# Kernel tuning notes

Measured on AMD Instinct MI355X. Metric: run time of the kernel, lower is better.

## Reference

```python
import jax, jax.numpy as jnp
import numpy as np

DIM = 1024      # input_size (C)
E = 8           # num_experts
TOPK = 2        # use_experts
MLP = 4 * DIM   # int(dim * mlp_ratio)
B, N = 4, 1024


def _gelu(v):
    # torch nn.GELU default = exact erf gelu
    return jax.nn.gelu(v, approximate=False)


def setup_inputs() -> dict:
    key = jax.random.key(0)
    ks = jax.random.split(key, 20)
    s = 0.02
    f32 = jnp.float32
    return {
        "x": jax.random.normal(ks[0], (B, N, DIM), f32),
        "prompt": jax.random.normal(ks[1], (B, N, DIM), f32),
        "t": jax.random.uniform(ks[2], (B, N, 1), f32) * 1000.0,
        # gating time_embedding MLP
        "te_w1": jax.random.normal(ks[3], (1, DIM), f32) * s,
        "te_b1": jnp.zeros((DIM,), f32),
        "te_w2": jax.random.normal(ks[4], (DIM, DIM), f32) * s,
        "te_b2": jnp.zeros((DIM,), f32),
        "gate_w": jax.random.normal(ks[5], (3 * DIM, E), f32) * s,
        # stacked per-expert params [E, ...]
        "ex_tw1": jax.random.normal(ks[6], (E, 1, DIM), f32) * s,
        "ex_tb1": jnp.zeros((E, DIM), f32),
        "ex_tw2": jax.random.normal(ks[7], (E, DIM, DIM), f32) * s,
        "ex_tb2": jnp.zeros((E, DIM), f32),
        "ex_mw1": jax.random.normal(ks[8], (E, 2 * DIM, MLP), f32) * s,
        "ex_mb1": jnp.zeros((E, MLP), f32),
        "ex_mw2": jax.random.normal(ks[9], (E, MLP, DIM), f32) * s,
        "ex_mb2": jnp.zeros((E, DIM), f32),
    }


def _forward(x, prompt, t, te_w1, te_b1, te_w2, te_b2, gate_w,
             ex_tw1, ex_tb1, ex_tw2, ex_tb2, ex_mw1, ex_mb1, ex_mw2, ex_mb2):
    Bb, Nn, C = x.shape
    xf = x.reshape(-1, C)            # [T, C]
    pf = prompt.reshape(-1, C)
    tf = t.reshape(-1, 1)            # [T, 1]
    T = xf.shape[0]

    # noisy_gate (eval: no noise)
    t_emb = _gelu(tf @ te_w1 + te_b1) @ te_w2 + te_b2          # [T, C]
    x_cat = jnp.concatenate([xf, pf, t_emb], axis=-1)          # [T, 3C]
    logits = x_cat @ gate_w                                    # [T, E]
    top_l, top_i = jax.lax.top_k(logits, TOPK)
    gates = jnp.zeros_like(logits).at[
        jnp.arange(T)[:, None], top_i
    ].set(jax.nn.softmax(top_l, axis=1))                       # [T, E]

    # per-expert diffusion MLP, dense over experts (gate==0 contributes 0,
    # identical math to dispatch/split/index_add combine)
    te = _gelu(jnp.einsum('to,eod->etd', tf, ex_tw1) + ex_tb1[:, None, :])
    te = jnp.einsum('etd,edf->etf', te, ex_tw2) + ex_tb2[:, None, :]   # [E,T,C]
    xc = jnp.concatenate([jnp.broadcast_to(xf, (E, T, C)), te], axis=-1)  # [E,T,2C]
    h = _gelu(jnp.einsum('etc,ech->eth', xc, ex_mw1) + ex_mb1[:, None, :])
    out_e = jnp.einsum('eth,ehd->etd', h, ex_mw2) + ex_mb2[:, None, :]    # [E,T,C]

    out_f = jnp.einsum('te,etd->td', gates, out_e)             # combine
    output = out_f.reshape(Bb, Nn, C)

    load = gates.sum(0)                                        # [E]
    eps = 1e-10
    bal = jnp.var(load, ddof=1) / (jnp.mean(load) ** 2 + eps)
    moe_loss = bal + bal  # weight_balance + load_balance (same argument)
    return output, moe_loss


def reference(x, prompt, t, te_w1, te_b1, te_w2, te_b2, gate_w,
              ex_tw1, ex_tb1, ex_tw2, ex_tb2, ex_mw1, ex_mb1, ex_mw2, ex_mb2):
    return _forward(x, prompt, t, te_w1, te_b1, te_w2, te_b2, gate_w,
                    ex_tw1, ex_tb1, ex_tw2, ex_tb2, ex_mw1, ex_mb1, ex_mw2, ex_mb2)
```

## Files before the change

kernel.cpp:

```cpp
#include <hip/hip_runtime.h>
#include <cmath>

#define TTOK 4096
#define CDIM 1024
#define NE 8
#define MLPD 4096
#define PCAP (2*TTOK + NE*128)

typedef __attribute__((ext_vector_type(8))) short short8;
typedef __attribute__((ext_vector_type(4))) float float4v;

__device__ __forceinline__ float bf2f(unsigned short h){
  return __uint_as_float(((unsigned int)h) << 16);
}
__device__ __forceinline__ unsigned short f2bf(float f){
  unsigned int u = __float_as_uint(f);
  u += 0x7FFFu + ((u >> 16) & 1u);
  return (unsigned short)(u >> 16);
}
__device__ __forceinline__ float gelu_exact(float x){
  return 0.5f * x * (1.0f + erff(x * 0.70710678118654752f));
}
__device__ __forceinline__ void gld16(const void* g, void* l){
  __builtin_amdgcn_global_load_lds((const __attribute__((address_space(1))) void*)g,
                                   (__attribute__((address_space(3))) void*)l, 16, 0, 0);
}

__global__ __launch_bounds__(256) void k_zero(float* out, int n, int* counts, float* loadsum){
  int i = blockIdx.x*256 + threadIdx.x;
  if (i < n) out[i] = 0.f;
  if (i < NE){ counts[i] = 0; loadsum[i] = 0.f; }
}

__global__ __launch_bounds__(256) void k_m2(const float* __restrict__ te_w2,
    const float* __restrict__ te_b2, const float* __restrict__ gate_w,
    float* __restrict__ M2, float* __restrict__ c2){
  int idx = blockIdx.x*256 + threadIdx.x;
  if (idx < CDIM*NE){
    int i = idx >> 3, e = idx & 7;
    float s = 0.f;
    for (int j = 0; j < CDIM; j++)
      s += te_w2[(size_t)i*CDIM + j] * gate_w[(size_t)(2*CDIM + j)*NE + e];
    M2[idx] = s;
  } else if (idx < CDIM*NE + NE){
    int e = idx - CDIM*NE;
    float s = 0.f;
    for (int j = 0; j < CDIM; j++)
      s += te_b2[j] * gate_w[(size_t)(2*CDIM + j)*NE + e];
    c2[e] = s;
  }
}

__global__ __launch_bounds__(256) void k_cvt_x(const float* __restrict__ x,
                                               unsigned short* __restrict__ xb, int n4){
  int i = blockIdx.x*256 + threadIdx.x;
  if (i >= n4) return;
  float4 v = reinterpret_cast<const float4*>(x)[i];
  ushort4 o;
  o.x = f2bf(v.x); o.y = f2bf(v.y); o.z = f2bf(v.z); o.w = f2bf(v.w);
  reinterpret_cast<ushort4*>(xb)[i] = o;
}

__global__ __launch_bounds__(256) void k_cvt_w(const float* __restrict__ W,
    unsigned short* __restrict__ Wt, int K, int N){
  __shared__ float tile[32][33];
  int kb = blockIdx.x*32, nb = blockIdx.y*32, e = blockIdx.z;
  const float* Wp = W + (size_t)e*K*N;
  unsigned short* Wo = Wt + (size_t)e*K*N;
  int tx = threadIdx.x & 31, ty = threadIdx.x >> 5;
  #pragma unroll
  for (int i = 0; i < 32; i += 8)
    tile[ty+i][tx] = Wp[(size_t)(kb+ty+i)*N + nb + tx];
  __syncthreads();
  #pragma unroll
  for (int i = 0; i < 32; i += 8)
    Wo[(size_t)(nb+ty+i)*K + kb + tx] = f2bf(tile[tx][ty+i]);
}

__global__ __launch_bounds__(256) void k_gate(const float* __restrict__ x,
    const float* __restrict__ p, const float* __restrict__ t,
    const float* __restrict__ te_w1, const float* __restrict__ te_b1,
    const float* __restrict__ gate_w, const float* __restrict__ M2,
    const float* __restrict__ c2,
    int* __restrict__ ti, float* __restrict__ tg,
    int* __restrict__ counts, float* __restrict__ loadsum){
  int tok = blockIdx.x, tid = threadIdx.x;
  float tv = t[tok];
  float acc[NE];
  #pragma unroll
  for (int e = 0; e < NE; e++) acc[e] = 0.f;
  for (int j = tid; j < CDIM; j += 256){
    float xv = x[(size_t)tok*CDIM + j];
    float pv = p[(size_t)tok*CDIM + j];
    float vv = gelu_exact(tv*te_w1[j] + te_b1[j]);
    const float* g0 = gate_w + (size_t)j*NE;
    const float* g1 = gate_w + (size_t)(CDIM + j)*NE;
    const float* m2 = M2 + (size_t)j*NE;
    #pragma unroll
    for (int e = 0; e < NE; e++) acc[e] += xv*g0[e] + pv*g1[e] + vv*m2[e];
  }
  __shared__ float red[256][NE];
  #pragma unroll
  for (int e = 0; e < NE; e++) red[tid][e] = acc[e];
  __syncthreads();
  for (int s = 128; s > 0; s >>= 1){
    if (tid < s){
      #pragma unroll
      for (int e = 0; e < NE; e++) red[tid][e] += red[tid+s][e];
    }
    __syncthreads();
  }
  if (tid == 0){
    float lg[NE];
    #pragma unroll
    for (int e = 0; e < NE; e++) lg[e] = red[0][e] + c2[e];
    int i1 = 0; float l1 = lg[0];
    #pragma unroll
    for (int e = 1; e < NE; e++) if (lg[e] > l1){ l1 = lg[e]; i1 = e; }
    int i2 = -1; float l2 = -3.4e38f;
    #pragma unroll
    for (int e = 0; e < NE; e++) if (e != i1 && lg[e] > l2){ l2 = lg[e]; i2 = e; }
    float ex  = expf(l2 - l1);
    float g1v = 1.f/(1.f + ex);
    float g2v = ex/(1.f + ex);
    ti[tok*2]   = i1; ti[tok*2+1] = i2;
    tg[tok*2]   = g1v; tg[tok*2+1] = g2v;
    atomicAdd(&counts[i1], 1);  atomicAdd(&counts[i2], 1);
    atomicAdd(&loadsum[i1], g1v); atomicAdd(&loadsum[i2], g2v);
  }
}

__global__ __launch_bounds__(256) void k_scan(const int* __restrict__ counts,
    int* __restrict__ poff, int* __restrict__ fillpos,
    int* __restrict__ tok_id, float* __restrict__ pgate, int* __restrict__ pe, int padg){
  __shared__ int so[NE+1];
  __shared__ int sc[NE];
  if (threadIdx.x == 0){
    int o = 0;
    for (int e = 0; e < NE; e++){
      so[e] = o; poff[e] = o; fillpos[e] = o;
      sc[e] = counts[e];
      o += (sc[e] + padg - 1) & ~(padg - 1);
    }
    so[NE] = o; poff[NE] = o;
  }
  __syncthreads();
  for (int e = 0; e < NE; e++){
    int s = so[e] + sc[e], en = so[e+1];
    for (int i = s + (int)threadIdx.x; i < en; i += 256){
      tok_id[i] = 0; pgate[i] = 0.f; pe[i] = e;
    }
  }
}

__global__ __launch_bounds__(256) void k_fill(const int* __restrict__ ti,
    const float* __restrict__ tg, int* __restrict__ fillpos,
    int* __restrict__ tok_id, float* __restrict__ pgate, int* __restrict__ pe){
  int tok = blockIdx.x*256 + threadIdx.x;
  if (tok >= TTOK) return;
  #pragma unroll
  for (int k = 0; k < 2; k++){
    int e = ti[tok*2 + k];
    int pos = atomicAdd(&fillpos[e], 1);
    tok_id[pos] = tok;
    pgate[pos]  = tg[tok*2 + k];
    pe[pos]     = e;
  }
}

__global__ __launch_bounds__(256) void k_vgelu(const float* __restrict__ t,
    const float* __restrict__ tw1, const float* __restrict__ tb1,
    const int* __restrict__ tok_id, const int* __restrict__ pe,
    const int* __restrict__ poff, unsigned short* __restrict__ vbuf){
  int idx = blockIdx.x*256 + threadIdx.x;
  int r = idx >> 10, k = idx & (CDIM - 1);
  if (r >= poff[NE]) return;
  int e = pe[r];
  float tv = t[tok_id[r]];
  float u = tv * tw1[(size_t)e*CDIM + k] + tb1[(size_t)e*CDIM + k];
  vbuf[(size_t)r*CDIM + k] = f2bf(gelu_exact(u));
}


__global__ __launch_bounds__(256,2) void k_mfma_te(
    const unsigned short* __restrict__ vbuf,
    const unsigned short* __restrict__ Wt1, const float* __restrict__ tb2,
    const int* __restrict__ poff, const int* __restrict__ pe,
    unsigned short* __restrict__ tebuf){
  __shared__ unsigned short As[128*32];
  __shared__ unsigned short Bs[128*32];
  int r0 = blockIdx.y * 128;
  if (r0 >= poff[NE]) return;
  int e = pe[r0];
  int n0 = blockIdx.x * 128;
  int tid = threadIdx.x, lane = tid & 63, w = tid >> 6;
  const unsigned short* Bp = Wt1 + (size_t)e*CDIM*CDIM;
  int mb = (w&1)*64, nb = (w>>1)*64;
  float4v acc[4][4];
  #pragma unroll
  for (int i=0;i<4;i++)
    #pragma unroll
    for (int j=0;j<4;j++) acc[i][j] = (float4v){0.f,0.f,0.f,0.f};
  int rowA = w*32 + (lane>>2);
  int ck = (lane&3)*8;
  for (int k0 = 0; k0 < CDIM; k0 += 32){
    __syncthreads();
    unsigned short* lA = As + (w*32)*32;
    unsigned short* lB = Bs + (w*32)*32;
    gld16(vbuf + (size_t)(r0+rowA)*CDIM + k0 + ck, lA);
    gld16(vbuf + (size_t)(r0+rowA+16)*CDIM + k0 + ck, lA + 16*32);
    gld16(Bp + (size_t)(n0+rowA)*CDIM + k0 + ck, lB);
    gld16(Bp + (size_t)(n0+rowA+16)*CDIM + k0 + ck, lB + 16*32);
    __syncthreads();
    short8 a[4], b[4];
    #pragma unroll
    for (int mi=0;mi<4;mi++) a[mi] = *(const short8*)(As + (mb+mi*16+(lane&15))*32 + (lane>>4)*8);
    #pragma unroll
    for (int ni=0;ni<4;ni++) b[ni] = *(const short8*)(Bs + (nb+ni*16+(lane&15))*32 + (lane>>4)*8);
    #pragma unroll
    for (int mi=0;mi<4;mi++)
      #pragma unroll
      for (int ni=0;ni<4;ni++)
        acc[mi][ni] = __builtin_amdgcn_mfma_f32_16x16x32_bf16(a[mi], b[ni], acc[mi][ni], 0, 0, 0);
  }
  int col = lane & 15, rq = (lane>>4)*4;
  const float* bias = tb2 + (size_t)e*CDIM + n0;
  #pragma unroll
  for (int mi=0;mi<4;mi++)
    #pragma unroll
    for (int ni=0;ni<4;ni++){
      int n = nb + ni*16 + col;
      #pragma unroll
      for (int rg=0;rg<4;rg++){
        int r = r0 + mb + mi*16 + rq + rg;
        tebuf[(size_t)r*CDIM + n0 + n] = f2bf(acc[mi][ni][rg] + bias[n]);
      }
    }
}

__global__ __launch_bounds__(256,2) void k_mfma_h(
    const unsigned short* __restrict__ xb, const unsigned short* __restrict__ tebuf,
    const unsigned short* __restrict__ Wt2, const float* __restrict__ mb1,
    const int* __restrict__ poff, const int* __restrict__ pe,
    const int* __restrict__ tok_id, unsigned short* __restrict__ hbuf){
  __shared__ unsigned short As[128*32];
  __shared__ unsigned short Bs[128*32];
  __shared__ int toks[128];
  int r0 = blockIdx.y * 128;
  if (r0 >= poff[NE]) return;
  int e = pe[r0];
  int n0 = blockIdx.x * 128;
  int tid = threadIdx.x, lane = tid & 63, w = tid >> 6;
  if (tid < 128) toks[tid] = tok_id[r0 + tid];
  const unsigned short* Bp = Wt2 + (size_t)e*(2*CDIM)*MLPD;
  int mb = (w&1)*64, nb = (w>>1)*64;
  float4v acc[4][4];
  #pragma unroll
  for (int i=0;i<4;i++)
    #pragma unroll
    for (int j=0;j<4;j++) acc[i][j] = (float4v){0.f,0.f,0.f,0.f};
  int rowA = w*32 + (lane>>2);
  int ck = (lane&3)*8;
  for (int k0 = 0; k0 < 2*CDIM; k0 += 32){
    __syncthreads();
    unsigned short* lA = As + (w*32)*32;
    unsigned short* lB = Bs + (w*32)*32;
    if (k0 < CDIM){
      int tok0 = toks[rowA], tok1 = toks[rowA+16];
      gld16(xb + (size_t)tok0*CDIM + k0 + ck, lA);
      gld16(xb + (size_t)tok1*CDIM + k0 + ck, lA + 16*32);
    } else {
      gld16(tebuf + (size_t)(r0+rowA)*CDIM + (k0-CDIM) + ck, lA);
      gld16(tebuf + (size_t)(r0+rowA+16)*CDIM + (k0-CDIM) + ck, lA + 16*32);
    }
    gld16(Bp + (size_t)(n0+rowA)*(2*CDIM) + k0 + ck, lB);
    gld16(Bp + (size_t)(n0+rowA+16)*(2*CDIM) + k0 + ck, lB + 16*32);
    __syncthreads();
    short8 a[4], b[4];
    #pragma unroll
    for (int mi=0;mi<4;mi++) a[mi] = *(const short8*)(As + (mb+mi*16+(lane&15))*32 + (lane>>4)*8);
    #pragma unroll
    for (int ni=0;ni<4;ni++) b[ni] = *(const short8*)(Bs + (nb+ni*16+(lane&15))*32 + (lane>>4)*8);
    #pragma unroll
    for (int mi=0;mi<4;mi++)
      #pragma unroll
      for (int ni=0;ni<4;ni++)
        acc[mi][ni] = __builtin_amdgcn_mfma_f32_16x16x32_bf16(a[mi], b[ni], acc[mi][ni], 0, 0, 0);
  }
  int col = lane & 15, rq = (lane>>4)*4;
  const float* bias = mb1 + (size_t)e*MLPD + n0;
  #pragma unroll
  for (int mi=0;mi<4;mi++)
    #pragma unroll
    for (int ni=0;ni<4;ni++){
      int n = nb + ni*16 + col;
      #pragma unroll
      for (int rg=0;rg<4;rg++){
        int r = r0 + mb + mi*16 + rq + rg;
        hbuf[(size_t)r*MLPD + n0 + n] = f2bf(gelu_exact(acc[mi][ni][rg] + bias[n]));
      }
    }
}

__global__ __launch_bounds__(256,2) void k_mfma_out(
    const unsigned short* __restrict__ hbuf,
    const unsigned short* __restrict__ Wt3, const float* __restrict__ mb2,
    const int* __restrict__ poff, const int* __restrict__ pe,
    const int* __restrict__ tok_id, const float* __restrict__ pgate,
    float* __restrict__ out){
  __shared__ unsigned short As[128*32];
  __shared__ unsigned short Bs[128*32];
  __shared__ int   toks[128];
  __shared__ float gts[128];
  int r0 = blockIdx.y * 128;
  if (r0 >= poff[NE]) return;
  int e = pe[r0];
  int n0 = blockIdx.x * 128;
  int tid = threadIdx.x, lane = tid & 63, w = tid >> 6;
  if (tid < 128){ toks[tid] = tok_id[r0 + tid]; gts[tid] = pgate[r0 + tid]; }
  const unsigned short* Bp = Wt3 + (size_t)e*MLPD*CDIM;
  int mb = (w&1)*64, nb = (w>>1)*64;
  float4v acc[4][4];
  #pragma unroll
  for (int i=0;i<4;i++)
    #pragma unroll
    for (int j=0;j<4;j++) acc[i][j] = (float4v){0.f,0.f,0.f,0.f};
  int rowA = w*32 + (lane>>2);
  int ck = (lane&3)*8;
  for (int k0 = 0; k0 < MLPD; k0 += 32){
    __syncthreads();
    unsigned short* lA = As + (w*32)*32;
    unsigned short* lB = Bs + (w*32)*32;
    gld16(hbuf + (size_t)(r0+rowA)*MLPD + k0 + ck, lA);
    gld16(hbuf + (size_t)(r0+rowA+16)*MLPD + k0 + ck, lA + 16*32);
    gld16(Bp + (size_t)(n0+rowA)*MLPD + k0 + ck, lB);
    gld16(Bp + (size_t)(n0+rowA+16)*MLPD + k0 + ck, lB + 16*32);
    __syncthreads();
    short8 a[4], b[4];
    #pragma unroll
    for (int mi=0;mi<4;mi++) a[mi] = *(const short8*)(As + (mb+mi*16+(lane&15))*32 + (lane>>4)*8);
    #pragma unroll
    for (int ni=0;ni<4;ni++) b[ni] = *(const short8*)(Bs + (nb+ni*16+(lane&15))*32 + (lane>>4)*8);
    #pragma unroll
    for (int mi=0;mi<4;mi++)
      #pragma unroll
      for (int ni=0;ni<4;ni++)
        acc[mi][ni] = __builtin_amdgcn_mfma_f32_16x16x32_bf16(a[mi], b[ni], acc[mi][ni], 0, 0, 0);
  }
  int col = lane & 15, rq = (lane>>4)*4;
  const float* bias = mb2 + (size_t)e*CDIM + n0;
  #pragma unroll
  for (int mi=0;mi<4;mi++)
    #pragma unroll
    for (int ni=0;ni<4;ni++){
      int n = nb + ni*16 + col;
      #pragma unroll
      for (int rg=0;rg<4;rg++){
        int rl = mb + mi*16 + rq + rg;
        float g = gts[rl];
        float val = acc[mi][ni][rg] + bias[n];
        atomicAdd(&out[(size_t)toks[rl]*CDIM + n0 + n], g*val);
      }
    }
}

__global__ __launch_bounds__(256) void k_gemm_te_f(
    const unsigned short* __restrict__ vbuf,
    const float* __restrict__ tw2, const float* __restrict__ tb2,
    const int* __restrict__ poff, const int* __restrict__ pe,
    unsigned short* __restrict__ tebuf){
  int r0 = blockIdx.y * 64;
  if (r0 >= poff[NE]) return;
  int e = pe[r0];
  int n0 = blockIdx.x * 64;
  const float* Bp = tw2 + (size_t)e*CDIM*CDIM;
  __shared__ float As[16][68];
  __shared__ float Bs[16][68];
  int tid = threadIdx.x;
  int tx = tid & 15, ty = tid >> 4;
  int lm = tid >> 2, lk = (tid & 3)*4;
  int bk = tid >> 4, bn = (tid & 15)*4;
  float acc[4][4] = {{0.f}};
  for (int k0 = 0; k0 < CDIM; k0 += 16){
    ushort4 av = *reinterpret_cast<const ushort4*>(vbuf + (size_t)(r0+lm)*CDIM + k0 + lk);
    float4  bv = *reinterpret_cast<const float4*>(Bp + (size_t)(k0+bk)*CDIM + n0 + bn);
    __syncthreads();
    As[lk+0][lm] = bf2f(av.x); As[lk+1][lm] = bf2f(av.y);
    As[lk+2][lm] = bf2f(av.z); As[lk+3][lm] = bf2f(av.w);
    *reinterpret_cast<float4*>(&Bs[bk][bn]) = bv;
    __syncthreads();
    #pragma unroll
    for (int k = 0; k < 16; k++){
      float4 a = *reinterpret_cast<const float4*>(&As[k][ty*4]);
      float4 b = *reinterpret_cast<const float4*>(&Bs[k][tx*4]);
      float am[4] = {a.x,a.y,a.z,a.w}, bn4[4] = {b.x,b.y,b.z,b.w};
      #pragma unroll
      for (int i = 0; i < 4; i++)
        #pragma unroll
        for (int j = 0; j < 4; j++) acc[i][j] += am[i]*bn4[j];
    }
  }
  #pragma unroll
  for (int i = 0; i < 4; i++){
    int r = r0 + ty*4 + i;
    #pragma unroll
    for (int j = 0; j < 4; j++){
      int n = n0 + tx*4 + j;
      tebuf[(size_t)r*CDIM + n] = f2bf(acc[i][j] + tb2[(size_t)e*CDIM + n]);
    }
  }
}

__global__ __launch_bounds__(256) void k_gemm_h_f(
    const float* __restrict__ x, const unsigned short* __restrict__ tebuf,
    const float* __restrict__ mw1, const float* __restrict__ mb1,
    const int* __restrict__ poff, const int* __restrict__ pe,
    const int* __restrict__ tok_id, unsigned short* __restrict__ hbuf){
  int r0 = blockIdx.y * 64;
  if (r0 >= poff[NE]) return;
  int e = pe[r0];
  int n0 = blockIdx.x * 64;
  const float* Bp = mw1 + (size_t)e*(2*CDIM)*MLPD;
  __shared__ float As[16][68];
  __shared__ float Bs[16][68];
  __shared__ int toks[64];
  int tid = threadIdx.x;
  if (tid < 64) toks[tid] = tok_id[r0 + tid];
  int tx = tid & 15, ty = tid >> 4;
  int lm = tid >> 2, lk = (tid & 3)*4;
  int bk = tid >> 4, bn = (tid & 15)*4;
  float acc[4][4] = {{0.f}};
  __syncthreads();
  for (int k0 = 0; k0 < 2*CDIM; k0 += 16){
    float4 af;
    if (k0 < CDIM){
      af = *reinterpret_cast<const float4*>(x + (size_t)toks[lm]*CDIM + k0 + lk);
    } else {
      ushort4 av = *reinterpret_cast<const ushort4*>(tebuf + (size_t)(r0+lm)*CDIM + (k0 - CDIM) + lk);
      af.x = bf2f(av.x); af.y = bf2f(av.y); af.z = bf2f(av.z); af.w = bf2f(av.w);
    }
    float4 bv = *reinterpret_cast<const float4*>(Bp + (size_t)(k0+bk)*MLPD + n0 + bn);
    __syncthreads();
    As[lk+0][lm] = af.x; As[lk+1][lm] = af.y;
    As[lk+2][lm] = af.z; As[lk+3][lm] = af.w;
    *reinterpret_cast<float4*>(&Bs[bk][bn]) = bv;
    __syncthreads();
    #pragma unroll
    for (int k = 0; k < 16; k++){
      float4 a = *reinterpret_cast<const float4*>(&As[k][ty*4]);
      float4 b = *reinterpret_cast<const float4*>(&Bs[k][tx*4]);
      float am[4] = {a.x,a.y,a.z,a.w}, bn4[4] = {b.x,b.y,b.z,b.w};
      #pragma unroll
      for (int i = 0; i < 4; i++)
        #pragma unroll
        for (int j = 0; j < 4; j++) acc[i][j] += am[i]*bn4[j];
    }
  }
  #pragma unroll
  for (int i = 0; i < 4; i++){
    int r = r0 + ty*4 + i;
    #pragma unroll
    for (int j = 0; j < 4; j++){
      int n = n0 + tx*4 + j;
      hbuf[(size_t)r*MLPD + n] = f2bf(gelu_exact(acc[i][j] + mb1[(size_t)e*MLPD + n]));
    }
  }
}

__global__ __launch_bounds__(256) void k_gemm_out_f(
    const unsigned short* __restrict__ hbuf,
    const float* __restrict__ mw2, const float* __restrict__ mb2,
    const int* __restrict__ poff, const int* __restrict__ pe,
    const int* __restrict__ tok_id, const float* __restrict__ pgate,
    float* __restrict__ out){
  int r0 = blockIdx.y * 64;
  if (r0 >= poff[NE]) return;
  int e = pe[r0];
  int n0 = blockIdx.x * 64;
  const float* Bp = mw2 + (size_t)e*MLPD*CDIM;
  __shared__ float As[16][68];
  __shared__ float Bs[16][68];
  __shared__ int   toks[64];
  __shared__ float gts[64];
  int tid = threadIdx.x;
  if (tid < 64){ toks[tid] = tok_id[r0 + tid]; gts[tid] = pgate[r0 + tid]; }
  int tx = tid & 15, ty = tid >> 4;
  int lm = tid >> 2, lk = (tid & 3)*4;
  int bk = tid >> 4, bn = (tid & 15)*4;
  float acc[4][4] = {{0.f}};
  __syncthreads();
  for (int k0 = 0; k0 < MLPD; k0 += 16){
    ushort4 av = *reinterpret_cast<const ushort4*>(hbuf + (size_t)(r0+lm)*MLPD + k0 + lk);
    float4  bv = *reinterpret_cast<const float4*>(Bp + (size_t)(k0+bk)*CDIM + n0 + bn);
    __syncthreads();
    As[lk+0][lm] = bf2f(av.x); As[lk+1][lm] = bf2f(av.y);
    As[lk+2][lm] = bf2f(av.z); As[lk+3][lm] = bf2f(av.w);
    *reinterpret_cast<float4*>(&Bs[bk][bn]) = bv;
    __syncthreads();
    #pragma unroll
    for (int k = 0; k < 16; k++){
      float4 a = *reinterpret_cast<const float4*>(&As[k][ty*4]);
      float4 b = *reinterpret_cast<const float4*>(&Bs[k][tx*4]);
      float am[4] = {a.x,a.y,a.z,a.w}, bn4[4] = {b.x,b.y,b.z,b.w};
      #pragma unroll
      for (int i = 0; i < 4; i++)
        #pragma unroll
        for (int j = 0; j < 4; j++) acc[i][j] += am[i]*bn4[j];
    }
  }
  #pragma unroll
  for (int i = 0; i < 4; i++){
    int rl = ty*4 + i;
    int tok = toks[rl];
    float g = gts[rl];
    #pragma unroll
    for (int j = 0; j < 4; j++){
      int n = n0 + tx*4 + j;
      float val = acc[i][j] + mb2[(size_t)e*CDIM + n];
      atomicAdd(&out[(size_t)tok*CDIM + n], g*val);
    }
  }
}

__global__ void k_loss(const float* __restrict__ loadsum, float* __restrict__ outp){
  if (threadIdx.x == 0 && blockIdx.x == 0){
    float m = 0.f;
    for (int e = 0; e < NE; e++) m += loadsum[e];
    m *= (1.f/NE);
    float v = 0.f;
    for (int e = 0; e < NE; e++){ float d = loadsum[e] - m; v += d*d; }
    v *= (1.f/(NE-1));
    float bal = v / (m*m + 1e-10f);
    outp[0] = 2.f * bal;
  }
}

extern "C" void kernel_launch(void* const* d_in, const int* in_sizes, int n_in,
                              void* d_out, int out_size, void* d_ws, size_t ws_size,
                              hipStream_t stream){
  const float* x      = (const float*)d_in[0];
  const float* p      = (const float*)d_in[1];
  const float* t      = (const float*)d_in[2];
  const float* te_w1  = (const float*)d_in[3];
  const float* te_b1  = (const float*)d_in[4];
  const float* te_w2  = (const float*)d_in[5];
  const float* te_b2  = (const float*)d_in[6];
  const float* gate_w = (const float*)d_in[7];
  const float* ex_tw1 = (const float*)d_in[8];
  const float* ex_tb1 = (const float*)d_in[9];
  const float* ex_tw2 = (const float*)d_in[10];
  const float* ex_tb2 = (const float*)d_in[11];
  const float* ex_mw1 = (const float*)d_in[12];
  const float* ex_mb1 = (const float*)d_in[13];
  const float* ex_mw2 = (const float*)d_in[14];
  const float* ex_mb2 = (const float*)d_in[15];
  float* out = (float*)d_out;

  char* ws = (char*)d_ws;
  size_t off = 0;
  auto take = [&](size_t b){ size_t r = off; off = (off + b + 255) & ~(size_t)255; return r; };
  int*   counts  = (int*)  (ws + take(NE*sizeof(int)));
  int*   fillpos = (int*)  (ws + take(NE*sizeof(int)));
  int*   poff    = (int*)  (ws + take((NE+1)*sizeof(int)));
  float* loadsum = (float*)(ws + take(NE*sizeof(float)));
  float* M2      = (float*)(ws + take((size_t)CDIM*NE*sizeof(float)));
  float* c2      = (float*)(ws + take(NE*sizeof(float)));
  int*   ti      = (int*)  (ws + take((size_t)TTOK*2*sizeof(int)));
  float* tg      = (float*)(ws + take((size_t)TTOK*2*sizeof(float)));
  int*   tok_id  = (int*)  (ws + take((size_t)PCAP*sizeof(int)));
  float* pgate   = (float*)(ws + take((size_t)PCAP*sizeof(float)));
  int*   pe      = (int*)  (ws + take((size_t)PCAP*sizeof(int)));

  size_t need_mfma = off
      + ((size_t)TTOK*CDIM*2 + 256)
      + ((size_t)PCAP*MLPD*2 + 256)
      + ((size_t)PCAP*CDIM*2 + 256)
      + ((size_t)NE*2*CDIM*MLPD*2 + 256);
  bool use_mfma = ws_size >= need_mfma;
  int padg = use_mfma ? 128 : 64;

  int nOut = TTOK*CDIM + 1;
  k_zero<<<dim3((nOut + 255)/256), dim3(256), 0, stream>>>(out, nOut, counts, loadsum);
  k_m2<<<dim3((CDIM*NE + NE + 255)/256), dim3(256), 0, stream>>>(te_w2, te_b2, gate_w, M2, c2);
  k_gate<<<dim3(TTOK), dim3(256), 0, stream>>>(x, p, t, te_w1, te_b1, gate_w, M2, c2,
                                               ti, tg, counts, loadsum);
  k_scan<<<dim3(1), dim3(256), 0, stream>>>(counts, poff, fillpos, tok_id, pgate, pe, padg);
  k_fill<<<dim3((TTOK + 255)/256), dim3(256), 0, stream>>>(ti, tg, fillpos, tok_id, pgate, pe);

  if (use_mfma){
    unsigned short* xb    = (unsigned short*)(ws + take((size_t)TTOK*CDIM*2));
    char*           hreg  = ws + take((size_t)PCAP*MLPD*2);
    unsigned short* vbuf  = (unsigned short*)hreg;
    unsigned short* Wt1   = (unsigned short*)(hreg + (size_t)PCAP*CDIM*2);
    unsigned short* hbuf  = (unsigned short*)hreg;
    unsigned short* tebuf = (unsigned short*)(ws + take((size_t)PCAP*CDIM*2));
    unsigned short* Wt2   = (unsigned short*)(ws + take((size_t)NE*2*CDIM*MLPD*2));
    unsigned short* Wt3   = Wt2;

    k_cvt_x<<<dim3((TTOK*CDIM/4 + 255)/256), dim3(256), 0, stream>>>(x, xb, TTOK*CDIM/4);
    k_cvt_w<<<dim3(CDIM/32, CDIM/32, NE), dim3(256), 0, stream>>>(ex_tw2, Wt1, CDIM, CDIM);
    k_cvt_w<<<dim3(2*CDIM/32, MLPD/32, NE), dim3(256), 0, stream>>>(ex_mw1, Wt2, 2*CDIM, MLPD);
    k_vgelu<<<dim3((PCAP*CDIM)/256), dim3(256), 0, stream>>>(t, ex_tw1, ex_tb1, tok_id, pe, poff, vbuf);
    k_mfma_te<<<dim3(CDIM/128, PCAP/128), dim3(256), 0, stream>>>(vbuf, Wt1, ex_tb2, poff, pe, tebuf);
    k_mfma_h<<<dim3(MLPD/128, PCAP/128), dim3(256), 0, stream>>>(xb, tebuf, Wt2, ex_mb1,
                                                                 poff, pe, tok_id, hbuf);
    k_cvt_w<<<dim3(MLPD/32, CDIM/32, NE), dim3(256), 0, stream>>>(ex_mw2, Wt3, MLPD, CDIM);
    k_mfma_out<<<dim3(CDIM/128, PCAP/128), dim3(256), 0, stream>>>(hbuf, Wt3, ex_mb2,
                                                                   poff, pe, tok_id, pgate, out);
  } else {
    unsigned short* vbuf  = (unsigned short*)(ws + take((size_t)PCAP*MLPD*2));
    unsigned short* hbuf  = vbuf;
    unsigned short* tebuf = (unsigned short*)(ws + take((size_t)PCAP*CDIM*2));
    k_vgelu<<<dim3((PCAP*CDIM)/256), dim3(256), 0, stream>>>(t, ex_tw1, ex_tb1, tok_id, pe, poff, vbuf);
    k_gemm_te_f<<<dim3(CDIM/64, PCAP/64), dim3(256), 0, stream>>>(vbuf, ex_tw2, ex_tb2, poff, pe, tebuf);
    k_gemm_h_f<<<dim3(MLPD/64, PCAP/64), dim3(256), 0, stream>>>(x, tebuf, ex_mw1, ex_mb1,
                                                                 poff, pe, tok_id, hbuf);
    k_gemm_out_f<<<dim3(CDIM/64, PCAP/64), dim3(256), 0, stream>>>(hbuf, ex_mw2, ex_mb2,
                                                                   poff, pe, tok_id, pgate, out);
  }
  k_loss<<<dim3(1), dim3(64), 0, stream>>>(loadsum, out + (size_t)TTOK*CDIM);
}
```

Measured before the change: 1.242 ms.

## Swizzle LDS fragments, fuse x conversion into gate, replace atomic combine

Adds an XOR-style rotation to the LDS layout used by the three MFMA GEMMs to cut bank conflicts on fragment reads. Folds the bf16 conversion of x into the gating kernel and widens the weight transpose-convert kernel to 64x64 tiles with vectorized loads and stores. Replaces the atomicAdd scatter in the output GEMM with plain stores into a per-slot buffer plus a separate gather-combine kernel that uses a position map. The trade-off is extra workspace for the output buffer and one more kernel launch.

```diff
diff --git a/kernel.cpp b/kernel.cpp
--- a/kernel.cpp
+++ b/kernel.cpp
@@ -8,6 +8,7 @@
 #define PCAP (2*TTOK + NE*128)
 
 typedef __attribute__((ext_vector_type(8))) short short8;
+typedef __attribute__((ext_vector_type(8))) unsigned short us8;
 typedef __attribute__((ext_vector_type(4))) float float4v;
 
 __device__ __forceinline__ float bf2f(unsigned short h){
@@ -24,6 +25,9 @@
 __device__ __forceinline__ void gld16(const void* g, void* l){
   __builtin_amdgcn_global_load_lds((const __attribute__((address_space(1))) void*)g,
                                    (__attribute__((address_space(3))) void*)l, 16, 0, 0);
+}
+__device__ __forceinline__ int frag_off(int m, int qf){
+  return (m*4 + ((qf + (m >> 1)) & 3)) << 3;
 }
 
 __global__ __launch_bounds__(256) void k_zero(float* out, int n, int* counts, float* loadsum){
@@ -51,30 +55,29 @@
   }
 }
 
-__global__ __launch_bounds__(256) void k_cvt_x(const float* __restrict__ x,
-                                               unsigned short* __restrict__ xb, int n4){
-  int i = blockIdx.x*256 + threadIdx.x;
-  if (i >= n4) return;
-  float4 v = reinterpret_cast<const float4*>(x)[i];
-  ushort4 o;
-  o.x = f2bf(v.x); o.y = f2bf(v.y); o.z = f2bf(v.z); o.w = f2bf(v.w);
-  reinterpret_cast<ushort4*>(xb)[i] = o;
-}
-
 __global__ __launch_bounds__(256) void k_cvt_w(const float* __restrict__ W,
     unsigned short* __restrict__ Wt, int K, int N){
-  __shared__ float tile[32][33];
-  int kb = blockIdx.x*32, nb = blockIdx.y*32, e = blockIdx.z;
-  const float* Wp = W + (size_t)e*K*N;
-  unsigned short* Wo = Wt + (size_t)e*K*N;
-  int tx = threadIdx.x & 31, ty = threadIdx.x >> 5;
-  #pragma unroll
-  for (int i = 0; i < 32; i += 8)
-    tile[ty+i][tx] = Wp[(size_t)(kb+ty+i)*N + nb + tx];
+  __shared__ unsigned short tile[64*66];
+  int kb = blockIdx.x*64, nb = blockIdx.y*64, e = blockIdx.z;
+  const float* Wp = W + (size_t)e*K*N + (size_t)kb*N + nb;
+  unsigned short* Wo = Wt + (size_t)e*K*N + (size_t)nb*K + kb;
+  int tid = threadIdx.x;
+  int kr = tid >> 4, nc = (tid & 15)*4;
+  #pragma unroll
+  for (int i = 0; i < 64; i += 16){
+    float4 v = *reinterpret_cast<const float4*>(Wp + (size_t)(kr + i)*N + nc);
+    unsigned short* d = &tile[(kr + i)*66 + nc];
+    d[0] = f2bf(v.x); d[1] = f2bf(v.y); d[2] = f2bf(v.z); d[3] = f2bf(v.w);
+  }
   __syncthreads();
-  #pragma unroll
-  for (int i = 0; i < 32; i += 8)
-    Wo[(size_t)(nb+ty+i)*K + kb + tx] = f2bf(tile[tx][ty+i]);
+  int nr = tid >> 2, kc = (tid & 3)*16;
+  #pragma unroll
+  for (int h = 0; h < 2; h++){
+    us8 o;
+    #pragma unroll
+    for (int j = 0; j < 8; j++) o[j] = tile[(kc + h*8 + j)*66 + nr];
+    *reinterpret_cast<us8*>(Wo + (size_t)nr*K + kc + h*8) = o;
+  }
 }
 
 __global__ __launch_bounds__(256) void k_gate(const float* __restrict__ x,
@@ -83,7 +86,8 @@
     const float* __restrict__ gate_w, const float* __restrict__ M2,
     const float* __restrict__ c2,
     int* __restrict__ ti, float* __restrict__ tg,
-    int* __restrict__ counts, float* __restrict__ loadsum){
+    int* __restrict__ counts, float* __restrict__ loadsum,
+    unsigned short* __restrict__ xb){
   int tok = blockIdx.x, tid = threadIdx.x;
   float tv = t[tok];
   float acc[NE];
@@ -92,6 +96,7 @@
   for (int j = tid; j < CDIM; j += 256){
     float xv = x[(size_t)tok*CDIM + j];
     float pv = p[(size_t)tok*CDIM + j];
+    if (xb) xb[(size_t)tok*CDIM + j] = f2bf(xv);
     float vv = gelu_exact(tv*te_w1[j] + te_b1[j]);
     const float* g0 = gate_w + (size_t)j*NE;
     const float* g1 = gate_w + (size_t)(CDIM + j)*NE;
@@ -155,7 +160,8 @@
 
 __global__ __launch_bounds__(256) void k_fill(const int* __restrict__ ti,
     const float* __restrict__ tg, int* __restrict__ fillpos,
-    int* __restrict__ tok_id, float* __restrict__ pgate, int* __restrict__ pe){
+    int* __restrict__ tok_id, float* __restrict__ pgate, int* __restrict__ pe,
+    int* __restrict__ posmap){
   int tok = blockIdx.x*256 + threadIdx.x;
   if (tok >= TTOK) return;
   #pragma unroll
@@ -165,6 +171,7 @@
     tok_id[pos] = tok;
     pgate[pos]  = tg[tok*2 + k];
     pe[pos]     = e;
+    posmap[tok*2 + k] = pos;
   }
 }
 
@@ -202,7 +209,8 @@
     #pragma unroll
     for (int j=0;j<4;j++) acc[i][j] = (float4v){0.f,0.f,0.f,0.f};
   int rowA = w*32 + (lane>>2);
-  int ck = (lane&3)*8;
+  int ck = (((lane & 3) - ((lane >> 3) & 3)) & 3) * 8;
+  int r15 = lane & 15, qf = lane >> 4;
   for (int k0 = 0; k0 < CDIM; k0 += 32){
     __syncthreads();
     unsigned short* lA = As + (w*32)*32;
@@ -214,9 +222,9 @@
     __syncthreads();
     short8 a[4], b[4];
     #pragma unroll
-    for (int mi=0;mi<4;mi++) a[mi] = *(const short8*)(As + (mb+mi*16+(lane&15))*32 + (lane>>4)*8);
-    #pragma unroll
-    for (int ni=0;ni<4;ni++) b[ni] = *(const short8*)(Bs + (nb+ni*16+(lane&15))*32 + (lane>>4)*8);
+    for (int mi=0;mi<4;mi++) a[mi] = *(const short8*)(As + frag_off(mb+mi*16+r15, qf));
+    #pragma unroll
+    for (int ni=0;ni<4;ni++) b[ni] = *(const short8*)(Bs + frag_off(nb+ni*16+r15, qf));
     #pragma unroll
     for (int mi=0;mi<4;mi++)
       #pragma unroll
@@ -260,7 +268,9 @@
     #pragma unroll
     for (int j=0;j<4;j++) acc[i][j] = (float4v){0.f,0.f,0.f,0.f};
   int rowA = w*32 + (lane>>2);
-  int ck = (lane&3)*8;
+  int ck = (((lane & 3) - ((lane >> 3) & 3)) & 3) * 8;
+  int r15 = lane & 15, qf = lane >> 4;
+  __syncthreads();
   for (int k0 = 0; k0 < 2*CDIM; k0 += 32){
     __syncthreads();
     unsigned short* lA = As + (w*32)*32;
@@ -278,9 +288,9 @@
     __syncthreads();
     short8 a[4], b[4];
     #pragma unroll
-    for (int mi=0;mi<4;mi++) a[mi] = *(const short8*)(As + (mb+mi*16+(lane&15))*32 + (lane>>4)*8);
-    #pragma unroll
-    for (int ni=0;ni<4;ni++) b[ni] = *(const short8*)(Bs + (nb+ni*16+(lane&15))*32 + (lane>>4)*8);
+    for (int mi=0;mi<4;mi++) a[mi] = *(const short8*)(As + frag_off(mb+mi*16+r15, qf));
+    #pragma unroll
+    for (int ni=0;ni<4;ni++) b[ni] = *(const short8*)(Bs + frag_off(nb+ni*16+r15, qf));
     #pragma unroll
     for (int mi=0;mi<4;mi++)
       #pragma unroll
@@ -306,18 +316,14 @@
     const unsigned short* __restrict__ hbuf,
     const unsigned short* __restrict__ Wt3, const float* __restrict__ mb2,
     const int* __restrict__ poff, const int* __restrict__ pe,
-    const int* __restrict__ tok_id, const float* __restrict__ pgate,
-    float* __restrict__ out){
+    float* __restrict__ obuf){
   __shared__ unsigned short As[128*32];
   __shared__ unsigned short Bs[128*32];
-  __shared__ int   toks[128];
-  __shared__ float gts[128];
   int r0 = blockIdx.y * 128;
   if (r0 >= poff[NE]) return;
   int e = pe[r0];
   int n0 = blockIdx.x * 128;
   int tid = threadIdx.x, lane = tid & 63, w = tid >> 6;
-  if (tid < 128){ toks[tid] = tok_id[r0 + tid]; gts[tid] = pgate[r0 + tid]; }
   const unsigned short* Bp = Wt3 + (size_t)e*MLPD*CDIM;
   int mb = (w&1)*64, nb = (w>>1)*64;
   float4v acc[4][4];
@@ -326,7 +332,8 @@
     #pragma unroll
     for (int j=0;j<4;j++) acc[i][j] = (float4v){0.f,0.f,0.f,0.f};
   int rowA = w*32 + (lane>>2);
-  int ck = (lane&3)*8;
+  int ck = (((lane & 3) - ((lane >> 3) & 3)) & 3) * 8;
+  int r15 = lane & 15, qf = lane >> 4;
   for (int k0 = 0; k0 < MLPD; k0 += 32){
     __syncthreads();
     unsigned short* lA = As + (w*32)*32;
@@ -338,9 +345,9 @@
     __syncthreads();
     short8 a[4], b[4];
     #pragma unroll
-    for (int mi=0;mi<4;mi++) a[mi] = *(const short8*)(As + (mb+mi*16+(lane&15))*32 + (lane>>4)*8);
-    #pragma unroll
-    for (int ni=0;ni<4;ni++) b[ni] = *(const short8*)(Bs + (nb+ni*16+(lane&15))*32 + (lane>>4)*8);
+    for (int mi=0;mi<4;mi++) a[mi] = *(const short8*)(As + frag_off(mb+mi*16+r15, qf));
+    #pragma unroll
+    for (int ni=0;ni<4;ni++) b[ni] = *(const short8*)(Bs + frag_off(nb+ni*16+r15, qf));
     #pragma unroll
     for (int mi=0;mi<4;mi++)
       #pragma unroll
@@ -356,12 +363,25 @@
       int n = nb + ni*16 + col;
       #pragma unroll
       for (int rg=0;rg<4;rg++){
-        int rl = mb + mi*16 + rq + rg;
-        float g = gts[rl];
-        float val = acc[mi][ni][rg] + bias[n];
-        atomicAdd(&out[(size_t)toks[rl]*CDIM + n0 + n], g*val);
+        int r = r0 + mb + mi*16 + rq + rg;
+        obuf[(size_t)r*CDIM + n0 + n] = acc[mi][ni][rg] + bias[n];
       }
     }
+}
+
+__global__ __launch_bounds__(256) void k_combine(const float* __restrict__ obuf,
+    const int* __restrict__ posmap, const float* __restrict__ tg,
+    float* __restrict__ out){
+  int idx = blockIdx.x*256 + threadIdx.x;
+  int tok = idx >> 8, n4 = (idx & 255)*4;
+  int p1 = posmap[tok*2], p2 = posmap[tok*2+1];
+  float g1 = tg[tok*2], g2 = tg[tok*2+1];
+  float4 a = *reinterpret_cast<const float4*>(obuf + (size_t)p1*CDIM + n4);
+  float4 b = *reinterpret_cast<const float4*>(obuf + (size_t)p2*CDIM + n4);
+  float4 o;
+  o.x = g1*a.x + g2*b.x; o.y = g1*a.y + g2*b.y;
+  o.z = g1*a.z + g2*b.z; o.w = g1*a.w + g2*b.w;
+  *reinterpret_cast<float4*>(out + (size_t)tok*CDIM + n4) = o;
 }
 
 __global__ __launch_bounds__(256) void k_gemm_te_f(
@@ -567,6 +587,7 @@
   float* c2      = (float*)(ws + take(NE*sizeof(float)));
   int*   ti      = (int*)  (ws + take((size_t)TTOK*2*sizeof(int)));
   float* tg      = (float*)(ws + take((size_t)TTOK*2*sizeof(float)));
+  int*   posmap  = (int*)  (ws + take((size_t)TTOK*2*sizeof(int)));
   int*   tok_id  = (int*)  (ws + take((size_t)PCAP*sizeof(int)));
   float* pgate   = (float*)(ws + take((size_t)PCAP*sizeof(float)));
   int*   pe      = (int*)  (ws + take((size_t)PCAP*sizeof(int)));
@@ -582,10 +603,6 @@
   int nOut = TTOK*CDIM + 1;
   k_zero<<<dim3((nOut + 255)/256), dim3(256), 0, stream>>>(out, nOut, counts, loadsum);
   k_m2<<<dim3((CDIM*NE + NE + 255)/256), dim3(256), 0, stream>>>(te_w2, te_b2, gate_w, M2, c2);
-  k_gate<<<dim3(TTOK), dim3(256), 0, stream>>>(x, p, t, te_w1, te_b1, gate_w, M2, c2,
-                                               ti, tg, counts, loadsum);
-  k_scan<<<dim3(1), dim3(256), 0, stream>>>(counts, poff, fillpos, tok_id, pgate, pe, padg);
-  k_fill<<<dim3((TTOK + 255)/256), dim3(256), 0, stream>>>(ti, tg, fillpos, tok_id, pgate, pe);
 
   if (use_mfma){
     unsigned short* xb    = (unsigned short*)(ws + take((size_t)TTOK*CDIM*2));
@@ -596,21 +613,30 @@
     unsigned short* tebuf = (unsigned short*)(ws + take((size_t)PCAP*CDIM*2));
     unsigned short* Wt2   = (unsigned short*)(ws + take((size_t)NE*2*CDIM*MLPD*2));
     unsigned short* Wt3   = Wt2;
-
-    k_cvt_x<<<dim3((TTOK*CDIM/4 + 255)/256), dim3(256), 0, stream>>>(x, xb, TTOK*CDIM/4);
-    k_cvt_w<<<dim3(CDIM/32, CDIM/32, NE), dim3(256), 0, stream>>>(ex_tw2, Wt1, CDIM, CDIM);
-    k_cvt_w<<<dim3(2*CDIM/32, MLPD/32, NE), dim3(256), 0, stream>>>(ex_mw1, Wt2, 2*CDIM, MLPD);
+    float*          obuf  = (float*)(Wt2 + (size_t)NE*MLPD*CDIM);
+
+    k_gate<<<dim3(TTOK), dim3(256), 0, stream>>>(x, p, t, te_w1, te_b1, gate_w, M2, c2,
+                                                 ti, tg, counts, loadsum, xb);
+    k_scan<<<dim3(1), dim3(256), 0, stream>>>(counts, poff, fillpos, tok_id, pgate, pe, padg);
+    k_fill<<<dim3((TTOK + 255)/256), dim3(256), 0, stream>>>(ti, tg, fillpos, tok_id, pgate, pe, posmap);
+    k_cvt_w<<<dim3(CDIM/64, CDIM/64, NE), dim3(256), 0, stream>>>(ex_tw2, Wt1, CDIM, CDIM);
+    k_cvt_w<<<dim3(2*CDIM/64, MLPD/64, NE), dim3(256), 0, stream>>>(ex_mw1, Wt2, 2*CDIM, MLPD);
     k_vgelu<<<dim3((PCAP*CDIM)/256), dim3(256), 0, stream>>>(t, ex_tw1, ex_tb1, tok_id, pe, poff, vbuf);
     k_mfma_te<<<dim3(CDIM/128, PCAP/128), dim3(256), 0, stream>>>(vbuf, Wt1, ex_tb2, poff, pe, tebuf);
     k_mfma_h<<<dim3(MLPD/128, PCAP/128), dim3(256), 0, stream>>>(xb, tebuf, Wt2, ex_mb1,
                                                                  poff, pe, tok_id, hbuf);
-    k_cvt_w<<<dim3(MLPD/32, CDIM/32, NE), dim3(256), 0, stream>>>(ex_mw2, Wt3, MLPD, CDIM);
+    k_cvt_w<<<dim3(MLPD/64, CDIM/64, NE), dim3(256), 0, stream>>>(ex_mw2, Wt3, MLPD, CDIM);
     k_mfma_out<<<dim3(CDIM/128, PCAP/128), dim3(256), 0, stream>>>(hbuf, Wt3, ex_mb2,
-                                                                   poff, pe, tok_id, pgate, out);
+                                                                   poff, pe, obuf);
+    k_combine<<<dim3((TTOK*CDIM/4)/256), dim3(256), 0, stream>>>(obuf, posmap, tg, out);
   } else {
     unsigned short* vbuf  = (unsigned short*)(ws + take((size_t)PCAP*MLPD*2));
     unsigned short* hbuf  = vbuf;
     unsigned short* tebuf = (unsigned short*)(ws + take((size_t)PCAP*CDIM*2));
+    k_gate<<<dim3(TTOK), dim3(256), 0, stream>>>(x, p, t, te_w1, te_b1, gate_w, M2, c2,
+                                                 ti, tg, counts, loadsum, (unsigned short*)nullptr);
+    k_scan<<<dim3(1), dim3(256), 0, stream>>>(counts, poff, fillpos, tok_id, pgate, pe, padg);
+    k_fill<<<dim3((TTOK + 255)/256), dim3(256), 0, stream>>>(ti, tg, fillpos, tok_id, pgate, pe, posmap);
     k_vgelu<<<dim3((PCAP*CDIM)/256), dim3(256), 0, stream>>>(t, ex_tw1, ex_tb1, tok_id, pe, poff, vbuf);
     k_gemm_te_f<<<dim3(CDIM/64, PCAP/64), dim3(256), 0, stream>>>(vbuf, ex_tw2, ex_tb2, poff, pe, tebuf);
     k_gemm_h_f<<<dim3(MLPD/64, PCAP/64), dim3(256), 0, stream>>>(x, tebuf, ex_mw1, ex_mb1,
```

Result: faster. 1.161 ms (-6.6%).
